# Kernel optimization log

Measured on AMD Instinct MI355X. Metric: run time of the kernel, lower is better.

Reference implementation:

```python
import jax, jax.numpy as jnp
import numpy as np

DIM = 1024
HEADS = 16
HEAD_DIM = DIM // HEADS
WINDOW = 512
NEG = -1e9  # matches masked_fill(-1e9) semantics; excluded keys get ~0 weight


def setup_inputs() -> dict:
    key = jax.random.key(0)
    ks = jax.random.split(key, 9)
    s = 1.0 / np.sqrt(DIM)
    inp = {"x": jax.random.normal(ks[0], (2, 4096, DIM), dtype=jnp.float32)}
    for i, name in enumerate(["q", "k", "v", "o"]):
        inp[f"W{name}"] = jax.random.uniform(ks[1 + 2 * i], (DIM, DIM), jnp.float32, -s, s)
        inp[f"b{name}"] = jax.random.uniform(ks[2 + 2 * i], (DIM,), jnp.float32, -s, s)
    return inp


def _sliding_window_attn(x, Wq, bq, Wk, bk, Wv, bv, Wo, bo):
    B, S, D = x.shape
    H, hd, W = HEADS, HEAD_DIM, WINDOW
    nb = S // W  # number of query blocks

    def proj(Wp, bp):
        y = x @ Wp.T + bp                       # [B,S,D]
        return y.reshape(B, S, H, hd).transpose(0, 2, 1, 3)  # [B,H,S,hd]

    q = proj(Wq, bq)
    k = proj(Wk, bk)
    v = proj(Wv, bv)

    scale = hd ** -0.5
    qb = q.reshape(B, H, nb, W, hd)

    def window_kv(t):
        # each query block n attends to blocks n-1 and n (2W keys)
        pad = jnp.concatenate([jnp.zeros((B, H, W, hd), t.dtype), t], axis=2)
        prev = pad[:, :, :S].reshape(B, H, nb, W, hd)
        cur = t.reshape(B, H, nb, W, hd)
        return jnp.concatenate([prev, cur], axis=3)  # [B,H,nb,2W,hd]

    kw = window_kv(k)
    vw = window_kv(v)

    scores = jnp.einsum('bhnqd,bhnkd->bhnqk', qb, kw) * scale  # [B,H,nb,W,2W]

    # key abs pos = n*W - W + t ; query abs pos = n*W + s
    t = jnp.arange(2 * W)            # [2W]
    s_ = jnp.arange(W)[:, None]      # [W,1]
    n = jnp.arange(nb)[:, None, None]  # [nb,1,1]
    valid = (t <= s_ + W) & (t >= s_ + 1) & (n * W - W + t >= 0)  # [nb,W,2W]
    scores = jnp.where(valid, scores, NEG)

    attn = jax.nn.softmax(scores, axis=-1)
    out = jnp.einsum('bhnqk,bhnkd->bhnqd', attn, vw)  # [B,H,nb,W,hd]
    out = out.reshape(B, H, S, hd).transpose(0, 2, 1, 3).reshape(B, S, D)
    return out @ Wo.T + bo


def reference(x, Wq, bq, Wk, bk, Wv, bv, Wo, bo):
    return _sliding_window_attn(x, Wq, bq, Wk, bk, Wv, bv, Wo, bo)
```

## Files before the change

kernel.cpp:

```cpp
#include <hip/hip_runtime.h>
#include <hip/hip_bf16.h>

typedef __bf16 bf16_t;
typedef __attribute__((ext_vector_type(8))) __bf16 bfrag;
typedef __attribute__((ext_vector_type(4))) __bf16 bf16x4;
typedef __attribute__((ext_vector_type(4))) float f32x4;

#define SEQ    4096
#define NDIM   1024
#define NHEAD  16
#define HD     64
#define NBATCH 2
#define MROWS  (NBATCH * SEQ)
#define LQK    2048
#define PSTR   76

__device__ __forceinline__ void gload_lds16(const bf16_t* g, bf16_t* l) {
    __builtin_amdgcn_global_load_lds(
        (const __attribute__((address_space(1))) unsigned int*)g,
        (__attribute__((address_space(3))) unsigned int*)l,
        16, 0, 0);
}

template <typename OT>
__global__ __launch_bounds__(256, 2)
void gemm_bt(const bf16_t* __restrict__ A, int lda,
             const bf16_t* __restrict__ W,
             const float* __restrict__ b0p, const float* __restrict__ b1p,
             const float* __restrict__ b2p, float qscale,
             OT* __restrict__ C, int ldc, int K,
             bf16_t* __restrict__ VtOut)
{
    __shared__ __align__(16) bf16_t As[128 * 32];
    __shared__ __align__(16) bf16_t Bs[128 * 32];

    const int tid  = threadIdx.x;
    const int lane = tid & 63;
    const int wid  = tid >> 6;
    const int n16  = lane & 15;
    const int quad = lane >> 4;
    const int row0 = blockIdx.y * 128;
    const int col0 = blockIdx.x * 128;
    const int wrow = (wid >> 1) * 64;
    const int wcol = (wid & 1) * 64;
    const float* bias = (col0 < 1024) ? b0p : (col0 < 2048 ? b1p : b2p);
    const float bsc = (col0 < 1024) ? qscale : 1.0f;
    const int bcol0 = col0 & 1023;

    f32x4 acc[4][4];
#pragma unroll
    for (int i = 0; i < 4; i++)
#pragma unroll
        for (int j = 0; j < 4; j++) acc[i][j] = (f32x4){0.f, 0.f, 0.f, 0.f};

    for (int k0 = 0; k0 < K; k0 += 32) {
#pragma unroll
        for (int it = 0; it < 2; it++) {
            int idx = tid + it * 256;
            int r   = idx >> 2;
            int c   = (idx & 3) * 8;
            gload_lds16(A + (size_t)(row0 + r) * lda + k0 + c, &As[(it * 256 + wid * 64) * 8]);
            gload_lds16(W + (size_t)(col0 + r) * K   + k0 + c, &Bs[(it * 256 + wid * 64) * 8]);
        }
        __syncthreads();

        bfrag af[4], bfg[4];
#pragma unroll
        for (int i = 0; i < 4; i++)
            af[i] = *(const bfrag*)(&As[(wrow + i * 16 + n16) * 32 + quad * 8]);
#pragma unroll
        for (int j = 0; j < 4; j++)
            bfg[j] = *(const bfrag*)(&Bs[(wcol + j * 16 + n16) * 32 + quad * 8]);

#pragma unroll
        for (int i = 0; i < 4; i++)
#pragma unroll
            for (int j = 0; j < 4; j++)
                acc[i][j] = __builtin_amdgcn_mfma_f32_16x16x32_bf16(af[i], bfg[j], acc[i][j], 0, 0, 0);
        __syncthreads();
    }

    if (col0 < 2048 || VtOut == nullptr) {
#pragma unroll
        for (int i = 0; i < 4; i++)
#pragma unroll
            for (int j = 0; j < 4; j++)
#pragma unroll
                for (int r = 0; r < 4; r++) {
                    int row = row0 + wrow + i * 16 + quad * 4 + r;
                    int col = wcol + j * 16 + n16;
                    float v = acc[i][j][r] + bias[bcol0 + col] * bsc;
                    C[(size_t)row * ldc + col0 + col] = (OT)v;
                }
    } else {
#pragma unroll
        for (int i = 0; i < 4; i++) {
#pragma unroll
            for (int j = 0; j < 4; j++) {
                int dg     = col0 + wcol + j * 16 + n16 - 2048;
                int token0 = row0 + wrow + i * 16 + quad * 4;
                int bb     = token0 >> 12;
                float bv   = bias[bcol0 + wcol + j * 16 + n16];
                size_t vrow = ((size_t)bb * NHEAD + (dg >> 6)) * HD + (dg & 63);
                bf16x4 pk;
#pragma unroll
                for (int r = 0; r < 4; r++) pk[r] = (__bf16)(acc[i][j][r] + bv);
                *(bf16x4*)&VtOut[vrow * SEQ + (token0 & (SEQ - 1))] = pk;
            }
        }
    }
}

__global__ __launch_bounds__(256)
void cast_x(const float* __restrict__ s, bf16_t* __restrict__ d)
{
    size_t i = ((size_t)blockIdx.x * 256 + threadIdx.x) * 8;
    float4 a = *(const float4*)(s + i);
    float4 b = *(const float4*)(s + i + 4);
    bfrag o;
    o[0] = (__bf16)a.x; o[1] = (__bf16)a.y; o[2] = (__bf16)a.z; o[3] = (__bf16)a.w;
    o[4] = (__bf16)b.x; o[5] = (__bf16)b.y; o[6] = (__bf16)b.z; o[7] = (__bf16)b.w;
    *(bfrag*)(d + i) = o;
}

__global__ __launch_bounds__(256)
void cast_w(const float* __restrict__ wq, const float* __restrict__ wk,
            const float* __restrict__ wv, const float* __restrict__ wo,
            bf16_t* __restrict__ d)
{
    size_t t   = (size_t)blockIdx.x * 256 + threadIdx.x;
    int    sel = (int)(t >> 17);
    const float* s = sel == 0 ? wq : (sel == 1 ? wk : (sel == 2 ? wv : wo));
    const float sc = (sel == 0) ? 0.125f : 1.0f;
    size_t off = (t & 131071) * 8;
    float4 a = *(const float4*)(s + off);
    float4 b = *(const float4*)(s + off + 4);
    bfrag o;
    o[0] = (__bf16)(a.x * sc); o[1] = (__bf16)(a.y * sc);
    o[2] = (__bf16)(a.z * sc); o[3] = (__bf16)(a.w * sc);
    o[4] = (__bf16)(b.x * sc); o[5] = (__bf16)(b.y * sc);
    o[6] = (__bf16)(b.z * sc); o[7] = (__bf16)(b.w * sc);
    *(bfrag*)(d + (size_t)sel * 1048576 + off) = o;
}

__global__ __launch_bounds__(256, 4)
void attn_win(const bf16_t* __restrict__ QK, const bf16_t* __restrict__ Vt,
              bf16_t* __restrict__ AO)
{
    __shared__ __align__(16) bf16_t Ks[2][64 * 72];
    __shared__ __align__(16) bf16_t Pw[4][32 * PSTR];

    const int tid  = threadIdx.x;
    const int wid  = tid >> 6;
    const int lane = tid & 63;
    const int n16  = lane & 15;
    const int quad = lane >> 4;

    const int lin = blockIdx.x;
    const int sub = lin >> 3;
    const int bh  = (lin & 7) * 4 + (sub >> 5);
    const int qt  = sub & 31;
    const int qb0 = qt * 128;

    const int b  = bh >> 4, h = bh & 15;
    const size_t bS   = (size_t)b * SEQ;
    const size_t hoff = (size_t)h * HD;
    const bf16_t* Vb  = Vt + (size_t)bh * HD * SEQ;
    const int wstart  = qb0 - 512;
    const int it0     = (qb0 < 512) ? ((512 - qb0) >> 6) : 0;

    const int srow  = tid >> 2;
    const int scol0 = (tid & 3) * 16;

    const int qwmin = qb0 + wid * 32;
    const int qwmax = qwmin + 31;
    int qa[2];
    bfrag bq0[2], bq1[2];
#pragma unroll
    for (int qg = 0; qg < 2; qg++) {
        qa[qg] = qwmin + qg * 16 + n16;
        bq0[qg] = *(const bfrag*)(&QK[(bS + qa[qg]) * LQK + hoff + quad * 8]);
        bq1[qg] = *(const bfrag*)(&QK[(bS + qa[qg]) * LQK + hoff + 32 + quad * 8]);
    }

    f32x4 ao[2][4];
#pragma unroll
    for (int qg = 0; qg < 2; qg++)
#pragma unroll
        for (int j = 0; j < 4; j++) ao[qg][j] = (f32x4){0.f, 0.f, 0.f, 0.f};
    float m[2] = {-1e30f, -1e30f}, l[2] = {0.f, 0.f};

    uint4 kp0, kp1;
    {
        const bf16_t* src = &QK[(bS + wstart + it0 * 64 + srow) * LQK + 1024 + hoff + scol0];
        kp0 = *(const uint4*)(src);
        kp1 = *(const uint4*)(src + 8);
    }

    for (int it = it0; it < 10; ++it) {
        const int k0 = wstart + it * 64;
        const int pb = it & 1;
        *(uint4*)(&Ks[pb][srow * 72 + scol0])     = kp0;
        *(uint4*)(&Ks[pb][srow * 72 + scol0 + 8]) = kp1;
        __syncthreads();
        if (it < 9) {
            const bf16_t* src = &QK[(bS + wstart + (it + 1) * 64 + srow) * LQK + 1024 + hoff + scol0];
            kp0 = *(const uint4*)(src);
            kp1 = *(const uint4*)(src + 8);
        }

        if (k0 > qwmax || k0 + 63 < qwmin - 511) continue;

        f32x4 a[2][4];
#pragma unroll
        for (int nt = 0; nt < 4; nt++) {
            bfrag ak0 = *(const bfrag*)(&Ks[pb][(nt * 16 + n16) * 72 + quad * 8]);
            bfrag ak1 = *(const bfrag*)(&Ks[pb][(nt * 16 + n16) * 72 + 32 + quad * 8]);
#pragma unroll
            for (int qg = 0; qg < 2; qg++) {
                f32x4 s4 = (f32x4){0.f, 0.f, 0.f, 0.f};
                s4 = __builtin_amdgcn_mfma_f32_16x16x32_bf16(ak0, bq0[qg], s4, 0, 0, 0);
                s4 = __builtin_amdgcn_mfma_f32_16x16x32_bf16(ak1, bq1[qg], s4, 0, 0, 0);
                a[qg][nt] = s4;
            }
        }

#pragma unroll
        for (int qg = 0; qg < 2; qg++) {
            const int gmin = qwmin + qg * 16, gmax = gmin + 15;
            const bool msk = !((k0 >= gmax - 511) & (k0 + 63 <= gmin));
            if (msk) {
#pragma unroll
                for (int nt = 0; nt < 4; nt++)
#pragma unroll
                    for (int r = 0; r < 4; r++) {
                        int ka = k0 + nt * 16 + quad * 4 + r;
                        bool valid = (ka >= qa[qg] - 511) & (ka <= qa[qg]);
                        if (!valid) a[qg][nt][r] = -1e30f;
                    }
            }

            float cm = -1e30f;
#pragma unroll
            for (int nt = 0; nt < 4; nt++)
#pragma unroll
                for (int r = 0; r < 4; r++) cm = fmaxf(cm, a[qg][nt][r]);
            cm = fmaxf(cm, __shfl_xor(cm, 16, 64));
            cm = fmaxf(cm, __shfl_xor(cm, 32, 64));
            float mn    = fmaxf(m[qg], cm);
            float alpha = __expf(m[qg] - mn);
            m[qg] = mn;
#pragma unroll
            for (int j = 0; j < 4; j++)
#pragma unroll
                for (int r = 0; r < 4; r++) ao[qg][j][r] *= alpha;

            float lacc = 0.f;
#pragma unroll
            for (int nt = 0; nt < 4; nt++) {
                bf16x4 pk;
#pragma unroll
                for (int r = 0; r < 4; r++) {
                    float p = __expf(a[qg][nt][r] - m[qg]);
                    lacc += p;
                    pk[r] = (__bf16)p;
                }
                *(bf16x4*)&Pw[wid][(qg * 16 + n16) * PSTR + nt * 16 + quad * 4] = pk;
            }
            l[qg] = l[qg] * alpha + lacc;
        }

#pragma unroll
        for (int ks = 0; ks < 2; ks++) {
            bfrag bp[2];
#pragma unroll
            for (int qg = 0; qg < 2; qg++)
                bp[qg] = *(const bfrag*)(&Pw[wid][(qg * 16 + n16) * PSTR + ks * 32 + quad * 8]);
#pragma unroll
            for (int j = 0; j < 4; j++) {
                bfrag av = *(const bfrag*)(&Vb[(size_t)(j * 16 + n16) * SEQ
                                               + k0 + ks * 32 + quad * 8]);
#pragma unroll
                for (int qg = 0; qg < 2; qg++)
                    ao[qg][j] = __builtin_amdgcn_mfma_f32_16x16x32_bf16(av, bp[qg], ao[qg][j], 0, 0, 0);
            }
        }
    }

#pragma unroll
    for (int qg = 0; qg < 2; qg++) {
        float lv = l[qg];
        lv += __shfl_xor(lv, 16, 64);
        lv += __shfl_xor(lv, 32, 64);
        const float inv = 1.0f / lv;
#pragma unroll
        for (int j = 0; j < 4; j++) {
            bf16x4 pk;
#pragma unroll
            for (int r = 0; r < 4; r++) pk[r] = (__bf16)(ao[qg][j][r] * inv);
            *(bf16x4*)&AO[(bS + qa[qg]) * NDIM + hoff + j * 16 + quad * 4] = pk;
        }
    }
}

extern "C" void kernel_launch(void* const* d_in, const int* in_sizes, int n_in,
                              void* d_out, int out_size, void* d_ws, size_t ws_size,
                              hipStream_t stream)
{
    const float* x  = (const float*)d_in[0];
    const float* Wq = (const float*)d_in[1];
    const float* bq = (const float*)d_in[2];
    const float* Wk = (const float*)d_in[3];
    const float* bk = (const float*)d_in[4];
    const float* Wv = (const float*)d_in[5];
    const float* bv = (const float*)d_in[6];
    const float* Wo = (const float*)d_in[7];
    const float* bo = (const float*)d_in[8];
    float* out = (float*)d_out;

    const size_t QK_E = (size_t)MROWS * LQK;
    const size_t X_E  = (size_t)MROWS * NDIM;
    if (ws_size < (QK_E + X_E + 4u * 1048576u) * sizeof(bf16_t)) return;

    bf16_t* QKb = (bf16_t*)d_ws;
    bf16_t* AbX = QKb + QK_E;
    bf16_t* Wc  = AbX + X_E;
    bf16_t* Wob = Wc + 3u * 1048576u;
    bf16_t* Vtg = (bf16_t*)d_out;

    dim3 blk(256);

    cast_x<<<dim3(4096), blk, 0, stream>>>(x, AbX);
    cast_w<<<dim3(2048), blk, 0, stream>>>(Wq, Wk, Wv, Wo, Wc);

    gemm_bt<bf16_t><<<dim3(3072 / 128, MROWS / 128), blk, 0, stream>>>(
        AbX, NDIM, Wc, bq, bk, bv, 0.125f, QKb, LQK, NDIM, Vtg);

    attn_win<<<dim3(1024), dim3(256), 0, stream>>>(QKb, Vtg, AbX);

    gemm_bt<float><<<dim3(NDIM / 128, MROWS / 128), blk, 0, stream>>>(
        AbX, NDIM, Wob, bo, bo, bo, 1.0f, out, NDIM, NDIM, nullptr);
}
```

Measured before the change: 269.6 us.

## Use 256x256-tile 512-thread pipelined GEMM for the QKV projection

Replaces the 128x128 QKV projection GEMM with a new 256x256-tile kernel using 8 waves. Staging uses direct global-to-LDS loads with an XOR swizzle and a split double-buffer schedule that prefetches A and B halves at different points, with setprio around the MFMA bursts. The larger tile raises arithmetic intensity and cuts global traffic. It uses 64KB of LDS and many accumulators, which risks lower occupancy. The grid drops to 12x32 blocks, which may underfill the CUs.

```diff
diff --git a/kernel.cpp b/kernel.cpp
--- a/kernel.cpp
+++ b/kernel.cpp
@@ -20,6 +20,151 @@
         (const __attribute__((address_space(1))) unsigned int*)g,
         (__attribute__((address_space(3))) unsigned int*)l,
         16, 0, 0);
+}
+
+__device__ __forceinline__ void block_sync() {
+    asm volatile("" ::: "memory");
+    __builtin_amdgcn_s_barrier();
+    asm volatile("" ::: "memory");
+}
+
+__device__ __forceinline__ void stage_half(const bf16_t* __restrict__ G, int ldg,
+                                           int grow0, int gk0, bf16_t* region,
+                                           int half, int tid)
+{
+    const int poff = half * 8192 + tid * 16;
+    const int loff = poff ^ (((poff >> 9) & 1) << 5);
+    const int r    = loff >> 6;
+    const int cb   = loff & 63;
+    const bf16_t* src = G + (size_t)(grow0 + r) * ldg + gk0 + (cb >> 1);
+    gload_lds16(src, region + ((half * 8192 + (tid >> 6) * 1024) >> 1));
+}
+
+__device__ __forceinline__ bfrag ldsfrag(const bf16_t* region, int R, int quad)
+{
+    const int off = (R * 64 + quad * 16) ^ (((R >> 3) & 1) << 5);
+    return *(const bfrag*)((const char*)region + off);
+}
+
+__global__ __launch_bounds__(512, 2)
+void gemm256(const bf16_t* __restrict__ A, int lda,
+             const bf16_t* __restrict__ W,
+             const float* __restrict__ b0p, const float* __restrict__ b1p,
+             const float* __restrict__ b2p, float qscale,
+             bf16_t* __restrict__ C, int ldc, int K,
+             bf16_t* __restrict__ VtOut)
+{
+    __shared__ __align__(1024) bf16_t LSD[32768];
+
+    const int tid  = threadIdx.x;
+    const int lane = tid & 63;
+    const int n16  = lane & 15;
+    const int quad = lane >> 4;
+    const int wm   = (tid >> 6) >> 2;
+    const int wn   = (tid >> 6) & 3;
+    const int row0 = blockIdx.y * 256;
+    const int col0 = blockIdx.x * 256;
+    const int nt   = K >> 5;
+
+    f32x4 acc[8][4];
+#pragma unroll
+    for (int m = 0; m < 8; m++)
+#pragma unroll
+        for (int j = 0; j < 4; j++) acc[m][j] = (f32x4){0.f, 0.f, 0.f, 0.f};
+
+    {
+        bf16_t* A0 = &LSD[0];
+        bf16_t* B0 = &LSD[8192];
+        bf16_t* B1 = &LSD[16384 + 8192];
+        stage_half(A, lda, row0, 0, A0, 0, tid);
+        stage_half(A, lda, row0, 0, A0, 1, tid);
+        stage_half(W, K, col0, 0, B0, 0, tid);
+        stage_half(W, K, col0, 0, B0, 1, tid);
+        stage_half(W, K, col0, 32, B1, 0, tid);
+        stage_half(W, K, col0, 32, B1, 1, tid);
+    }
+    asm volatile("s_waitcnt vmcnt(2)" ::: "memory");
+
+    for (int t = 0; t < nt; ++t) {
+        bf16_t* Ab  = &LSD[(t & 1) * 16384];
+        bf16_t* Bb  = Ab + 8192;
+        bf16_t* AbN = &LSD[((t & 1) ^ 1) * 16384];
+
+        bfrag a[4], b[4];
+
+        block_sync();
+#pragma unroll
+        for (int m = 0; m < 4; m++) a[m] = ldsfrag(Ab, wm * 128 + m * 16 + n16, quad);
+#pragma unroll
+        for (int j = 0; j < 4; j++) b[j] = ldsfrag(Bb, wn * 64 + j * 16 + n16, quad);
+        if (t + 1 < nt) {
+            stage_half(A, lda, row0, (t + 1) * 32, AbN, 0, tid);
+            stage_half(A, lda, row0, (t + 1) * 32, AbN, 1, tid);
+        }
+        asm volatile("s_waitcnt lgkmcnt(0)" ::: "memory");
+        __builtin_amdgcn_sched_barrier(0);
+        __builtin_amdgcn_s_setprio(1);
+#pragma unroll
+        for (int m = 0; m < 4; m++)
+#pragma unroll
+            for (int j = 0; j < 4; j++)
+                acc[m][j] = __builtin_amdgcn_mfma_f32_16x16x32_bf16(a[m], b[j], acc[m][j], 0, 0, 0);
+        __builtin_amdgcn_s_setprio(0);
+
+        block_sync();
+#pragma unroll
+        for (int m = 0; m < 4; m++) a[m] = ldsfrag(Ab, wm * 128 + (m + 4) * 16 + n16, quad);
+        if (t + 2 < nt) {
+            stage_half(W, K, col0, (t + 2) * 32, Bb, 0, tid);
+            stage_half(W, K, col0, (t + 2) * 32, Bb, 1, tid);
+        }
+        asm volatile("s_waitcnt lgkmcnt(0)" ::: "memory");
+        __builtin_amdgcn_sched_barrier(0);
+        __builtin_amdgcn_s_setprio(1);
+#pragma unroll
+        for (int m = 0; m < 4; m++)
+#pragma unroll
+            for (int j = 0; j < 4; j++)
+                acc[m + 4][j] = __builtin_amdgcn_mfma_f32_16x16x32_bf16(a[m], b[j], acc[m + 4][j], 0, 0, 0);
+        __builtin_amdgcn_s_setprio(0);
+
+        if (t < nt - 2) asm volatile("s_waitcnt vmcnt(2)" ::: "memory");
+        else            asm volatile("s_waitcnt vmcnt(0)" ::: "memory");
+    }
+
+    const float* bias = (col0 < 1024) ? b0p : (col0 < 2048 ? b1p : b2p);
+    const float bsc   = (col0 < 1024) ? qscale : 1.0f;
+    const int bcol0   = col0 & 1023;
+
+    if (col0 < 2048 || VtOut == nullptr) {
+#pragma unroll
+        for (int m = 0; m < 8; m++)
+#pragma unroll
+            for (int j = 0; j < 4; j++)
+#pragma unroll
+                for (int r = 0; r < 4; r++) {
+                    int row = row0 + wm * 128 + m * 16 + quad * 4 + r;
+                    int col = wn * 64 + j * 16 + n16;
+                    float v = acc[m][j][r] + bias[bcol0 + col] * bsc;
+                    C[(size_t)row * ldc + col0 + col] = (bf16_t)v;
+                }
+    } else {
+#pragma unroll
+        for (int m = 0; m < 8; m++) {
+#pragma unroll
+            for (int j = 0; j < 4; j++) {
+                int dg     = col0 + wn * 64 + j * 16 + n16 - 2048;
+                int token0 = row0 + wm * 128 + m * 16 + quad * 4;
+                int bb     = token0 >> 12;
+                float bv   = bias[bcol0 + wn * 64 + j * 16 + n16];
+                size_t vrow = ((size_t)bb * NHEAD + (dg >> 6)) * HD + (dg & 63);
+                bf16x4 pk;
+#pragma unroll
+                for (int r = 0; r < 4; r++) pk[r] = (__bf16)(acc[m][j][r] + bv);
+                *(bf16x4*)&VtOut[vrow * SEQ + (token0 & (SEQ - 1))] = pk;
+            }
+        }
+    }
 }
 
 template <typename OT>
@@ -333,7 +478,7 @@
     cast_x<<<dim3(4096), blk, 0, stream>>>(x, AbX);
     cast_w<<<dim3(2048), blk, 0, stream>>>(Wq, Wk, Wv, Wo, Wc);
 
-    gemm_bt<bf16_t><<<dim3(3072 / 128, MROWS / 128), blk, 0, stream>>>(
+    gemm256<<<dim3(3072 / 256, MROWS / 256), dim3(512), 0, stream>>>(
         AbX, NDIM, Wc, bq, bk, bv, 0.125f, QKb, LQK, NDIM, Vtg);
 
     attn_win<<<dim3(1024), dim3(256), 0, stream>>>(QKb, Vtg, AbX);
```

After: 269.9 us. Within noise of the previous version (+0.1%).

## Replace GEMM with double-buffered 256-row tile kernel using swizzled LDS

Applied to the files above, without the earlier changes.

Replaces the simple 128x128 single-buffered bf16 GEMM with a 512-thread kernel using 256xBN tiles. It double-buffers A and B in LDS, issuing global-to-LDS loads for the next k-step while the current one runs MFMAs. It also XOR-swizzles LDS to avoid bank conflicts, remaps workgroups for L2 locality, and raises wave priority around the MFMA blocks. The goal is to hide global memory latency and raise MFMA utilization in the QKV and output projections. The cost is more registers and LDS per block, plus hand-placed waitcnt/barrier ordering that could be fragile.

```diff
diff --git a/kernel.cpp b/kernel.cpp
--- a/kernel.cpp
+++ b/kernel.cpp
@@ -22,89 +22,159 @@
         16, 0, 0);
 }
 
-template <typename OT>
-__global__ __launch_bounds__(256, 2)
-void gemm_bt(const bf16_t* __restrict__ A, int lda,
+__device__ __forceinline__ void block_sync() {
+    asm volatile("" ::: "memory");
+    __builtin_amdgcn_s_barrier();
+    asm volatile("" ::: "memory");
+}
+#define VMC(n)  asm volatile("s_waitcnt vmcnt(" #n ")" ::: "memory")
+
+__device__ __forceinline__ void stage_half(const bf16_t* __restrict__ G, int ldg,
+                                           int grow0, int gk0, bf16_t* region,
+                                           int half, int tid)
+{
+    const int poff = half * 8192 + tid * 16;
+    const int loff = poff ^ (((poff >> 9) & 1) << 5);
+    const int r    = loff >> 6;
+    const int cb   = loff & 63;
+    const bf16_t* src = G + (size_t)(grow0 + r) * ldg + gk0 + (cb >> 1);
+    gload_lds16(src, region + ((half * 8192 + (tid >> 6) * 1024) >> 1));
+}
+
+__device__ __forceinline__ bfrag ldsfrag(const bf16_t* region, int R, int quad)
+{
+    const int off = (R * 64 + quad * 16) ^ (((R >> 3) & 1) << 5);
+    return *(const bfrag*)((const char*)region + off);
+}
+
+template <int BN, typename OT>
+__global__ __launch_bounds__(512, 2)
+void gemm2ph(const bf16_t* __restrict__ A, int lda,
              const bf16_t* __restrict__ W,
              const float* __restrict__ b0p, const float* __restrict__ b1p,
              const float* __restrict__ b2p, float qscale,
              OT* __restrict__ C, int ldc, int K,
-             bf16_t* __restrict__ VtOut)
-{
-    __shared__ __align__(16) bf16_t As[128 * 32];
-    __shared__ __align__(16) bf16_t Bs[128 * 32];
+             bf16_t* __restrict__ VtOut, int nbx)
+{
+    constexpr int JR   = BN / 64;
+    constexpr int NBH  = BN / 128;
+    constexpr int ABUF = 8192;
+    constexpr int BBUF = BN * 32;
+    constexpr int BUF  = ABUF + BBUF;
+    __shared__ __align__(1024) bf16_t LSD[2 * BUF];
 
     const int tid  = threadIdx.x;
     const int lane = tid & 63;
-    const int wid  = tid >> 6;
     const int n16  = lane & 15;
     const int quad = lane >> 4;
-    const int row0 = blockIdx.y * 128;
-    const int col0 = blockIdx.x * 128;
-    const int wrow = (wid >> 1) * 64;
-    const int wcol = (wid & 1) * 64;
+    const int wid  = tid >> 6;
+    const int wm   = wid >> 2;
+    const int wn   = wid & 3;
+
+    const int nwg = (int)gridDim.x;
+    const int f   = (int)blockIdx.x;
+    const int swz = (f & 7) * (nwg >> 3) + (f >> 3);
+    const int bx  = swz % nbx;
+    const int by  = swz / nbx;
+    const int row0 = by * 256;
+    const int col0 = bx * BN;
+    const int nt   = K >> 5;
+
+    f32x4 acc[8][JR];
+#pragma unroll
+    for (int m = 0; m < 8; m++)
+#pragma unroll
+        for (int j = 0; j < JR; j++) acc[m][j] = (f32x4){0.f, 0.f, 0.f, 0.f};
+
+    {
+        bf16_t* A0 = &LSD[0];
+        bf16_t* B0 = &LSD[ABUF];
+        bf16_t* B1 = &LSD[BUF + ABUF];
+        stage_half(A, lda, row0, 0, A0, 0, tid);
+        stage_half(A, lda, row0, 0, A0, 1, tid);
+        stage_half(W, K, col0, 0, B0, 0, tid);
+        if constexpr (NBH == 2) stage_half(W, K, col0, 0, B0, 1, tid);
+        stage_half(W, K, col0, 32, B1, 0, tid);
+        if constexpr (NBH == 2) stage_half(W, K, col0, 32, B1, 1, tid);
+    }
+    if constexpr (NBH == 2) { VMC(2); } else { VMC(1); }
+
+    for (int t = 0; t < nt; ++t) {
+        bf16_t* Ab  = &LSD[(t & 1) * BUF];
+        bf16_t* Bb  = Ab + ABUF;
+        bf16_t* AbN = &LSD[((t & 1) ^ 1) * BUF];
+
+        bfrag a[4], b[JR];
+
+        block_sync();
+#pragma unroll
+        for (int m = 0; m < 4; m++) a[m] = ldsfrag(Ab, wm * 128 + m * 16 + n16, quad);
+#pragma unroll
+        for (int j = 0; j < JR; j++) b[j] = ldsfrag(Bb, wn * (BN / 4) + j * 16 + n16, quad);
+        if (t + 1 < nt) {
+            stage_half(A, lda, row0, (t + 1) * 32, AbN, 0, tid);
+            stage_half(A, lda, row0, (t + 1) * 32, AbN, 1, tid);
+        }
+        asm volatile("s_waitcnt lgkmcnt(0)" ::: "memory");
+        __builtin_amdgcn_sched_barrier(0);
+        __builtin_amdgcn_s_setprio(1);
+#pragma unroll
+        for (int m = 0; m < 4; m++)
+#pragma unroll
+            for (int j = 0; j < JR; j++)
+                acc[m][j] = __builtin_amdgcn_mfma_f32_16x16x32_bf16(a[m], b[j], acc[m][j], 0, 0, 0);
+        __builtin_amdgcn_s_setprio(0);
+
+        block_sync();
+#pragma unroll
+        for (int m = 0; m < 4; m++) a[m] = ldsfrag(Ab, wm * 128 + (m + 4) * 16 + n16, quad);
+        if (t + 2 < nt) {
+            stage_half(W, K, col0, (t + 2) * 32, Bb, 0, tid);
+            if constexpr (NBH == 2) stage_half(W, K, col0, (t + 2) * 32, Bb, 1, tid);
+        }
+        asm volatile("s_waitcnt lgkmcnt(0)" ::: "memory");
+        __builtin_amdgcn_sched_barrier(0);
+        __builtin_amdgcn_s_setprio(1);
+#pragma unroll
+        for (int m = 0; m < 4; m++)
+#pragma unroll
+            for (int j = 0; j < JR; j++)
+                acc[m + 4][j] = __builtin_amdgcn_mfma_f32_16x16x32_bf16(a[m], b[j], acc[m + 4][j], 0, 0, 0);
+        __builtin_amdgcn_s_setprio(0);
+
+        if (t < nt - 2) { if constexpr (NBH == 2) { VMC(2); } else { VMC(1); } }
+        else            { VMC(0); }
+    }
+
     const float* bias = (col0 < 1024) ? b0p : (col0 < 2048 ? b1p : b2p);
-    const float bsc = (col0 < 1024) ? qscale : 1.0f;
-    const int bcol0 = col0 & 1023;
-
-    f32x4 acc[4][4];
-#pragma unroll
-    for (int i = 0; i < 4; i++)
-#pragma unroll
-        for (int j = 0; j < 4; j++) acc[i][j] = (f32x4){0.f, 0.f, 0.f, 0.f};
-
-    for (int k0 = 0; k0 < K; k0 += 32) {
-#pragma unroll
-        for (int it = 0; it < 2; it++) {
-            int idx = tid + it * 256;
-            int r   = idx >> 2;
-            int c   = (idx & 3) * 8;
-            gload_lds16(A + (size_t)(row0 + r) * lda + k0 + c, &As[(it * 256 + wid * 64) * 8]);
-            gload_lds16(W + (size_t)(col0 + r) * K   + k0 + c, &Bs[(it * 256 + wid * 64) * 8]);
-        }
-        __syncthreads();
-
-        bfrag af[4], bfg[4];
-#pragma unroll
-        for (int i = 0; i < 4; i++)
-            af[i] = *(const bfrag*)(&As[(wrow + i * 16 + n16) * 32 + quad * 8]);
-#pragma unroll
-        for (int j = 0; j < 4; j++)
-            bfg[j] = *(const bfrag*)(&Bs[(wcol + j * 16 + n16) * 32 + quad * 8]);
-
-#pragma unroll
-        for (int i = 0; i < 4; i++)
-#pragma unroll
-            for (int j = 0; j < 4; j++)
-                acc[i][j] = __builtin_amdgcn_mfma_f32_16x16x32_bf16(af[i], bfg[j], acc[i][j], 0, 0, 0);
-        __syncthreads();
-    }
+    const float bsc   = (col0 < 1024) ? qscale : 1.0f;
+    const int bcol0   = col0 & 1023;
 
     if (col0 < 2048 || VtOut == nullptr) {
 #pragma unroll
-        for (int i = 0; i < 4; i++)
-#pragma unroll
-            for (int j = 0; j < 4; j++)
+        for (int m = 0; m < 8; m++)
+#pragma unroll
+            for (int j = 0; j < JR; j++)
 #pragma unroll
                 for (int r = 0; r < 4; r++) {
-                    int row = row0 + wrow + i * 16 + quad * 4 + r;
-                    int col = wcol + j * 16 + n16;
-                    float v = acc[i][j][r] + bias[bcol0 + col] * bsc;
+                    int row = row0 + wm * 128 + m * 16 + quad * 4 + r;
+                    int col = wn * (BN / 4) + j * 16 + n16;
+                    float v = acc[m][j][r] + bias[bcol0 + col] * bsc;
                     C[(size_t)row * ldc + col0 + col] = (OT)v;
                 }
     } else {
 #pragma unroll
-        for (int i = 0; i < 4; i++) {
-#pragma unroll
-            for (int j = 0; j < 4; j++) {
-                int dg     = col0 + wcol + j * 16 + n16 - 2048;
-                int token0 = row0 + wrow + i * 16 + quad * 4;
+        for (int m = 0; m < 8; m++) {
+#pragma unroll
+            for (int j = 0; j < JR; j++) {
+                int dg     = col0 + wn * (BN / 4) + j * 16 + n16 - 2048;
+                int token0 = row0 + wm * 128 + m * 16 + quad * 4;
                 int bb     = token0 >> 12;
-                float bv   = bias[bcol0 + wcol + j * 16 + n16];
+                float bv   = bias[bcol0 + wn * (BN / 4) + j * 16 + n16];
                 size_t vrow = ((size_t)bb * NHEAD + (dg >> 6)) * HD + (dg & 63);
                 bf16x4 pk;
 #pragma unroll
-                for (int r = 0; r < 4; r++) pk[r] = (__bf16)(acc[i][j][r] + bv);
+                for (int r = 0; r < 4; r++) pk[r] = (__bf16)(acc[m][j][r] + bv);
                 *(bf16x4*)&VtOut[vrow * SEQ + (token0 & (SEQ - 1))] = pk;
             }
         }
@@ -333,11 +403,11 @@
     cast_x<<<dim3(4096), blk, 0, stream>>>(x, AbX);
     cast_w<<<dim3(2048), blk, 0, stream>>>(Wq, Wk, Wv, Wo, Wc);
 
-    gemm_bt<bf16_t><<<dim3(3072 / 128, MROWS / 128), blk, 0, stream>>>(
-        AbX, NDIM, Wc, bq, bk, bv, 0.125f, QKb, LQK, NDIM, Vtg);
+    gemm2ph<256, bf16_t><<<dim3(384), dim3(512), 0, stream>>>(
+        AbX, NDIM, Wc, bq, bk, bv, 0.125f, QKb, LQK, NDIM, Vtg, 12);
 
     attn_win<<<dim3(1024), dim3(256), 0, stream>>>(QKb, Vtg, AbX);
 
-    gemm_bt<float><<<dim3(NDIM / 128, MROWS / 128), blk, 0, stream>>>(
-        AbX, NDIM, Wob, bo, bo, bo, 1.0f, out, NDIM, NDIM, nullptr);
-}
+    gemm2ph<128, float><<<dim3(256), dim3(512), 0, stream>>>(
+        AbX, NDIM, Wob, bo, bo, bo, 1.0f, out, NDIM, NDIM, nullptr, 8);
+}
```

Result: no change. 265.8 us (-1.4%).
